# Kernel optimization log

Measured on AMD Instinct MI355X. Metric: run time of the kernel, lower is better.

The kernel has to match this reference:

```python
import jax, jax.numpy as jnp
import numpy as np

B, H, S, D = 8, 16, 1024, 64

def setup_inputs() -> dict:
    key = jax.random.key(0)
    kq, kk, kv, km = jax.random.split(key, 4)
    Q = jax.random.normal(kq, (B, H, S, D), dtype=jnp.float32)
    K = jax.random.normal(kk, (B, H, S, D), dtype=jnp.float32)
    V = jax.random.normal(kv, (B, H, S, D), dtype=jnp.float32)
    attn_mask = jax.random.randint(km, (B, H, S, S), 0, 2).astype(bool)
    return {"Q": Q, "K": K, "V": V, "attn_mask": attn_mask}

def reference(Q, K, V, attn_mask):
    # scores = Q @ K^T  (NOTE: source has no 1/sqrt(d) scaling)
    scores = jnp.einsum("bhqd,bhkd->bhqk", Q, K)
    # source uses masked_fill_(mask, 1e-9), i.e. masked positions become 1e-9 (not -inf)
    scores = jnp.where(attn_mask, jnp.float32(1e-9), scores)
    attn = jax.nn.softmax(scores, axis=-1)
    context = jnp.einsum("bhqk,bhkd->bhqd", attn, V)
    return context, attn
```

## Files before the change

### kernel.cpp

```cpp
#include <hip/hip_runtime.h>

#define Sn 1024
#define Dn 64
#define PH_LD 1032
#define K_LD 72
#define V_LD 72

typedef short v8s __attribute__((ext_vector_type(8)));
typedef unsigned short v8u __attribute__((ext_vector_type(8)));
typedef float v4f __attribute__((ext_vector_type(4)));
typedef int   v4i __attribute__((ext_vector_type(4)));

#define LGKM0()  asm volatile("s_waitcnt lgkmcnt(0)" ::: "memory")
#define SBAR()   do { asm volatile("" ::: "memory"); __builtin_amdgcn_s_barrier(); \
                      __builtin_amdgcn_sched_barrier(0); } while (0)

__device__ __forceinline__ unsigned short f2bf(float x) {
    union { float f; unsigned u; } v; v.f = x;
    return (unsigned short)((v.u + 0x7FFFu + ((v.u >> 16) & 1u)) >> 16);
}
__device__ __forceinline__ float bf2f(unsigned short h) {
    union { float f; unsigned u; } v; v.u = ((unsigned)h) << 16;
    return v.f;
}
__device__ __forceinline__ void split2(float x, unsigned short& h, unsigned short& l) {
    unsigned short hs = f2bf(x);
    h = hs; l = f2bf(x - bf2f(hs));
}

__global__ __launch_bounds__(256) void prep_kf(const float* __restrict__ K,
    unsigned short* __restrict__ KF)
{
    const int bh = blockIdx.x >> 4, kt = blockIdx.x & 15;
    const int t = threadIdx.x;
    const int w = t >> 6, lane = t & 63;
    const int fr = lane & 15, g = lane >> 4;
    const float* src = K + (((size_t)(bh << 10) + (kt << 6) + (w << 4) + fr) << 6);
    const v4f a0 = __builtin_nontemporal_load((const v4f*)(src + (g << 3)));
    const v4f a1 = __builtin_nontemporal_load((const v4f*)(src + (g << 3) + 4));
    const v4f b0 = __builtin_nontemporal_load((const v4f*)(src + 32 + (g << 3)));
    const v4f b1 = __builtin_nontemporal_load((const v4f*)(src + 32 + (g << 3) + 4));
    v8u h0, h1, l0, l1;
    #pragma unroll
    for (int j = 0; j < 4; ++j) {
        unsigned short hh, ll;
        split2(a0[j], hh, ll); h0[j] = hh;     l0[j] = ll;
        split2(a1[j], hh, ll); h0[4 + j] = hh; l0[4 + j] = ll;
        split2(b0[j], hh, ll); h1[j] = hh;     l1[j] = ll;
        split2(b1[j], hh, ll); h1[4 + j] = hh; l1[4 + j] = ll;
    }
    unsigned short* dst = KF + ((size_t)bh << 17) + ((size_t)((kt << 2) + w) << 11) + (lane << 3);
    *(v8u*)(dst)        = h0;
    *(v8u*)(dst + 512)  = h1;
    *(v8u*)(dst + 1024) = l0;
    *(v8u*)(dst + 1536) = l1;
}

__global__ __launch_bounds__(256) void prep_vf(const float* __restrict__ V,
    unsigned short* __restrict__ VF)
{
    __shared__ float Ts[64][65];
    const int bh = blockIdx.x >> 4, kt = blockIdx.x & 15;
    const int t = threadIdx.x;
    {
        const int r = t >> 2, cs = (t & 3) << 4;
        const float* src = V + ((size_t)bh * Sn + (kt << 6) + r) * Dn + cs;
        const v4f a = __builtin_nontemporal_load((const v4f*)src);
        const v4f b = __builtin_nontemporal_load((const v4f*)src + 1);
        const v4f c = __builtin_nontemporal_load((const v4f*)src + 2);
        const v4f d = __builtin_nontemporal_load((const v4f*)src + 3);
        #pragma unroll
        for (int j = 0; j < 4; ++j) {
            Ts[r][cs + j]      = a[j];
            Ts[r][cs + 4 + j]  = b[j];
            Ts[r][cs + 8 + j]  = c[j];
            Ts[r][cs + 12 + j] = d[j];
        }
    }
    __syncthreads();
    {
        const int w = t >> 6, lane = t & 63;
        const int fr = lane & 15, g = lane >> 4;
        const int d = (w << 4) + fr;
        unsigned short* dst = VF + ((size_t)bh << 16) + ((size_t)((kt << 2) + w) << 10) + (lane << 3);
        v8u o0, o1;
        #pragma unroll
        for (int j = 0; j < 8; ++j) o0[j] = f2bf(Ts[(g << 3) + j][d]);
        #pragma unroll
        for (int j = 0; j < 8; ++j) o1[j] = f2bf(Ts[32 + (g << 3) + j][d]);
        *(v8u*)dst         = o0;
        *(v8u*)(dst + 512) = o1;
    }
}

__global__ __launch_bounds__(256) void prep_m(const int* __restrict__ M,
    unsigned long long* __restrict__ MW)
{
    const int NW = 2097152;
    const int lane = threadIdx.x & 63;
    const int wave = (blockIdx.x << 2) + (threadIdx.x >> 6);
    const int nwaves = gridDim.x << 2;
    for (int w0 = wave << 3; w0 < NW; w0 += nwaves << 3) {
        unsigned long long b[8];
        #pragma unroll
        for (int s = 0; s < 8; ++s) {
            const int v = __builtin_nontemporal_load(&M[((size_t)(w0 + s) << 6) + lane]);
            b[s] = __ballot(v != 0);
        }
        if (lane == 0) {
            ulonglong2* dst = (ulonglong2*)(MW + w0);
            ulonglong2 p0, p1, p2, p3;
            p0.x = b[0]; p0.y = b[1]; p1.x = b[2]; p1.y = b[3];
            p2.x = b[4]; p2.y = b[5]; p3.x = b[6]; p3.y = b[7];
            dst[0] = p0; dst[1] = p1; dst[2] = p2; dst[3] = p3;
        }
    }
}

__global__ __launch_bounds__(256, 4) void fused_attn_c(
    const unsigned short* __restrict__ KFG, const unsigned short* __restrict__ VFG,
    const float* __restrict__ Q, const unsigned long long* __restrict__ MW,
    float* __restrict__ attnO, float* __restrict__ ctxO)
{
    __shared__ unsigned short Ph[16][PH_LD];
    __shared__ float rsumW[4][16];
    __shared__ float invL[16];

    const int tid  = threadIdx.x;
    const int lane = tid & 63;
    const int w    = tid >> 6;
    const int fr   = lane & 15;
    const int g    = lane >> 4;

    const int swz = ((blockIdx.x & 7) << 10) + (blockIdx.x >> 3);
    const int bh = swz >> 6;
    const int q0 = (swz & 63) << 4;

    const float* Qb = Q + (size_t)bh * Sn * Dn + (size_t)q0 * Dn;
    float*       Ab = attnO + (size_t)bh * Sn * Sn + (size_t)q0 * Sn;
    float*       Cb = ctxO  + (size_t)bh * Sn * Dn + (size_t)q0 * Dn;
    const unsigned short* KFb = KFG + ((size_t)bh << 17);
    const unsigned short* VFb = VFG + ((size_t)bh << 16);
    const unsigned long long* mwp = MW + ((size_t)bh << 14) + ((size_t)(q0 + fr) << 4);

    v8s qh0, qh1, ql0, ql1;
    {
        const float* qp = Qb + fr * Dn + (g << 3);
        float x0[8], x1[8];
        *(v4f*)&x0[0] = *(const v4f*)qp;
        *(v4f*)&x0[4] = *(const v4f*)(qp + 4);
        *(v4f*)&x1[0] = *(const v4f*)(qp + 32);
        *(v4f*)&x1[4] = *(const v4f*)(qp + 36);
        #pragma unroll
        for (int i = 0; i < 8; ++i) {
            unsigned short hh, ll;
            split2(x0[i], hh, ll); qh0[i] = (short)hh; ql0[i] = (short)ll;
            split2(x1[i], hh, ll); qh1[i] = (short)hh; ql1[i] = (short)ll;
        }
    }

    const int sh = (w << 4) + (g << 2);

#define LDK(kt, h0, h1, l0, l1) do {                                               \
        const unsigned short* _p = KFb + ((size_t)(((kt) << 2) + w) << 11) + (lane << 3); \
        h0 = *(const v8s*)_p;          h1 = *(const v8s*)(_p + 512);               \
        l0 = *(const v8s*)(_p + 1024); l1 = *(const v8s*)(_p + 1536);              \
    } while (0)

#define STEPA(h0, h1, l0, l1, mwv, kt) do {                                        \
        v4f acc = {0.f, 0.f, 0.f, 0.f};                                            \
        __builtin_amdgcn_s_setprio(1);                                             \
        acc = __builtin_amdgcn_mfma_f32_16x16x32_bf16(h0, qh0, acc, 0, 0, 0);      \
        acc = __builtin_amdgcn_mfma_f32_16x16x32_bf16(h1, qh1, acc, 0, 0, 0);      \
        acc = __builtin_amdgcn_mfma_f32_16x16x32_bf16(l0, qh0, acc, 0, 0, 0);      \
        acc = __builtin_amdgcn_mfma_f32_16x16x32_bf16(l1, qh1, acc, 0, 0, 0);      \
        acc = __builtin_amdgcn_mfma_f32_16x16x32_bf16(h0, ql0, acc, 0, 0, 0);      \
        acc = __builtin_amdgcn_mfma_f32_16x16x32_bf16(h1, ql1, acc, 0, 0, 0);      \
        __builtin_amdgcn_s_setprio(0);                                             \
        const unsigned mb = (unsigned)((mwv) >> sh);                               \
        const float e0 = (mb & 1u) ? 1.0f : __expf(acc[0]);                        \
        const float e1 = (mb & 2u) ? 1.0f : __expf(acc[1]);                        \
        const float e2 = (mb & 4u) ? 1.0f : __expf(acc[2]);                        \
        const float e3 = (mb & 8u) ? 1.0f : __expf(acc[3]);                        \
        rs += (e0 + e1) + (e2 + e3);                                               \
        ushort4 pk;                                                                \
        pk.x = f2bf(e0); pk.y = f2bf(e1); pk.z = f2bf(e2); pk.w = f2bf(e3);        \
        *(ushort4*)&Ph[fr][((kt) << 6) + (w << 4) + (g << 2)] = pk;                \
    } while (0)

    float rs = 0.f;

    {
        v8s ah0, ah1, al0, al1, bh0, bh1, bl0, bl1;
        LDK(0, ah0, ah1, al0, al1);
        LDK(1, bh0, bh1, bl0, bl1);
        unsigned long long mA = mwp[0], mB = mwp[1];
        for (int kt = 0; kt < 16; kt += 2) {
            const int k2 = (kt + 2 < 16) ? kt + 2 : kt;
            const int k3 = (kt + 3 < 16) ? kt + 3 : kt;
            v8s ch0, ch1, cl0, cl1, dh0, dh1, dl0, dl1;
            LDK(k2, ch0, ch1, cl0, cl1);
            LDK(k3, dh0, dh1, dl0, dl1);
            const unsigned long long mC = mwp[k2];
            const unsigned long long mD = mwp[k3];
            STEPA(ah0, ah1, al0, al1, mA, kt);
            STEPA(bh0, bh1, bl0, bl1, mB, kt + 1);
            ah0 = ch0; ah1 = ch1; al0 = cl0; al1 = cl1; mA = mC;
            bh0 = dh0; bh1 = dh1; bl0 = dl0; bl1 = dl1; mB = mD;
        }
    }

    rs += __shfl_xor(rs, 16);
    rs += __shfl_xor(rs, 32);
    if (g == 0) rsumW[w][fr] = rs;
    __builtin_amdgcn_sched_barrier(0);
    LGKM0();
    SBAR();
    if (tid < 16) {
        const float s = rsumW[0][tid] + rsumW[1][tid] + rsumW[2][tid] + rsumW[3][tid];
        invL[tid] = 1.0f / s;
    }
    __builtin_amdgcn_sched_barrier(0);
    LGKM0();
    SBAR();

#define LDV(kt, v0, v1) do {                                                       \
        const unsigned short* _p = VFb + ((size_t)(((kt) << 2) + w) << 10) + (lane << 3); \
        v0 = *(const v8s*)_p;  v1 = *(const v8s*)(_p + 512);                       \
    } while (0)

#define STEPB(v0, v1, kt) do {                                                     \
        const v8s a0 = *(const v8s*)&Ph[fr][((kt) << 6) + (g << 3)];               \
        const v8s a1 = *(const v8s*)&Ph[fr][((kt) << 6) + 32 + (g << 3)];          \
        __builtin_amdgcn_s_setprio(1);                                             \
        accp = __builtin_amdgcn_mfma_f32_16x16x32_bf16(a0, v0, accp, 0, 0, 0);     \
        accp = __builtin_amdgcn_mfma_f32_16x16x32_bf16(a1, v1, accp, 0, 0, 0);     \
        __builtin_amdgcn_s_setprio(0);                                             \
    } while (0)

    v8s va0, va1, vb0, vb1;
    LDV(0, va0, va1);
    LDV(1, vb0, vb1);

    {
        const int qq = tid >> 4, ii = tid & 15;
        const float inv = invL[qq];
        float* arow = Ab + (size_t)qq * Sn;
        #pragma unroll
        for (int c = 0; c < 16; ++c) {
            const int k0 = (c << 6) + (ii << 2);
            const ushort4 p = *(const ushort4*)&Ph[qq][k0];
            v4f o;
            o[0] = bf2f(p.x) * inv; o[1] = bf2f(p.y) * inv;
            o[2] = bf2f(p.z) * inv; o[3] = bf2f(p.w) * inv;
            __builtin_nontemporal_store(o, (v4f*)(arow + k0));
        }
    }

    const int dcol = (w << 4) + fr;
    v4f accp = {0.f, 0.f, 0.f, 0.f};
    for (int kt = 0; kt < 16; kt += 2) {
        const int k2 = (kt + 2 < 16) ? kt + 2 : kt;
        const int k3 = (kt + 3 < 16) ? kt + 3 : kt;
        v8s vc0, vc1, vd0, vd1;
        LDV(k2, vc0, vc1);
        LDV(k3, vd0, vd1);
        STEPB(va0, va1, kt);
        STEPB(vb0, vb1, kt + 1);
        va0 = vc0; va1 = vc1;
        vb0 = vd0; vb1 = vd1;
    }
    #pragma unroll
    for (int r = 0; r < 4; ++r) {
        const int q = (g << 2) + r;
        __builtin_nontemporal_store(accp[r] * invL[q], &Cb[(size_t)q * Dn + dcol]);
    }
#undef LDK
#undef STEPA
#undef LDV
#undef STEPB
}

__global__ __launch_bounds__(256, 3) void fused_attn_fb(
    const float* __restrict__ Q, const float* __restrict__ K,
    const float* __restrict__ V, const int* __restrict__ M,
    float* __restrict__ attnO, float* __restrict__ ctxO)
{
    __shared__ unsigned short Ph[16][1048];
    __shared__ __align__(16) unsigned short Kraw[2 * 64 * K_LD];
    __shared__ float rsumW[4][16];
    __shared__ float invL[16];

    unsigned short (*Khi)[K_LD] = (unsigned short (*)[K_LD])Kraw;
    unsigned short (*Klo)[K_LD] = (unsigned short (*)[K_LD])(Kraw + 64 * K_LD);
    unsigned short (*Vt)[V_LD]  = (unsigned short (*)[V_LD])Kraw;

    const int tid  = threadIdx.x;
    const int lane = tid & 63;
    const int w    = tid >> 6;
    const int fr   = lane & 15;
    const int g    = lane >> 4;

    const int bh = blockIdx.x >> 6;
    const int q0 = (blockIdx.x & 63) << 4;

    const float* Qb = Q + (size_t)bh * Sn * Dn + (size_t)q0 * Dn;
    const float* Kb = K + (size_t)bh * Sn * Dn;
    const float* Vb = V + (size_t)bh * Sn * Dn;
    const int*   Mb = M + (size_t)bh * Sn * Sn + (size_t)q0 * Sn;
    float*       Ab = attnO + (size_t)bh * Sn * Sn + (size_t)q0 * Sn;
    float*       Cb = ctxO  + (size_t)bh * Sn * Dn + (size_t)q0 * Dn;

    v8s qh0, qh1, ql0, ql1;
    {
        const float* qp = Qb + fr * Dn + (g << 3);
        float x0[8], x1[8];
        *(v4f*)&x0[0] = *(const v4f*)qp;
        *(v4f*)&x0[4] = *(const v4f*)(qp + 4);
        *(v4f*)&x1[0] = *(const v4f*)(qp + 32);
        *(v4f*)&x1[4] = *(const v4f*)(qp + 36);
        #pragma unroll
        for (int i = 0; i < 8; ++i) {
            unsigned short hh, ll;
            split2(x0[i], hh, ll); qh0[i] = (short)hh; ql0[i] = (short)ll;
            split2(x1[i], hh, ll); qh1[i] = (short)hh; ql1[i] = (short)ll;
        }
    }

    const int srow = tid >> 4;
    const int sc4  = (tid & 15) << 2;

    const int* mp = Mb + (size_t)fr * Sn + (w << 4) + (g << 2);
    v4i mv = *(const v4i*)mp;

    v4f ka[4];
    #pragma unroll
    for (int i = 0; i < 4; ++i)
        ka[i] = *(const v4f*)(Kb + (size_t)(srow + (i << 4)) * Dn + sc4);

    float rs = 0.f;

    for (int kt = 0; kt < 16; ++kt) {
        __syncthreads();
        v4f kb[4];
        if (kt < 15) {
            const float* kn = Kb + (size_t)((kt + 1) << 6) * Dn;
            #pragma unroll
            for (int i = 0; i < 4; ++i)
                kb[i] = *(const v4f*)(kn + (size_t)(srow + (i << 4)) * Dn + sc4);
        }
        v4i mnext = mv;
        if (kt < 15) mnext = *(const v4i*)(mp + ((kt + 1) << 6));

        #pragma unroll
        for (int i = 0; i < 4; ++i) {
            const int row = srow + (i << 4);
            ushort4 hv, lv;
            split2(ka[i][0], hv.x, lv.x); split2(ka[i][1], hv.y, lv.y);
            split2(ka[i][2], hv.z, lv.z); split2(ka[i][3], hv.w, lv.w);
            *(ushort4*)&Khi[row][sc4] = hv;
            *(ushort4*)&Klo[row][sc4] = lv;
        }
        __syncthreads();

        const int krow = (w << 4) + fr;
        const v8s kh0 = *(const v8s*)&Khi[krow][(g << 3)];
        const v8s kh1 = *(const v8s*)&Khi[krow][32 + (g << 3)];
        const v8s kl0 = *(const v8s*)&Klo[krow][(g << 3)];
        const v8s kl1 = *(const v8s*)&Klo[krow][32 + (g << 3)];

        v4f acc = {0.f, 0.f, 0.f, 0.f};
        acc = __builtin_amdgcn_mfma_f32_16x16x32_bf16(kh0, qh0, acc, 0, 0, 0);
        acc = __builtin_amdgcn_mfma_f32_16x16x32_bf16(kh1, qh1, acc, 0, 0, 0);
        acc = __builtin_amdgcn_mfma_f32_16x16x32_bf16(kl0, qh0, acc, 0, 0, 0);
        acc = __builtin_amdgcn_mfma_f32_16x16x32_bf16(kl1, qh1, acc, 0, 0, 0);
        acc = __builtin_amdgcn_mfma_f32_16x16x32_bf16(kh0, ql0, acc, 0, 0, 0);
        acc = __builtin_amdgcn_mfma_f32_16x16x32_bf16(kh1, ql1, acc, 0, 0, 0);

        const float e0 = mv[0] ? 1.0f : __expf(acc[0]);
        const float e1 = mv[1] ? 1.0f : __expf(acc[1]);
        const float e2 = mv[2] ? 1.0f : __expf(acc[2]);
        const float e3 = mv[3] ? 1.0f : __expf(acc[3]);
        rs += (e0 + e1) + (e2 + e3);
        ushort4 pk;
        pk.x = f2bf(e0); pk.y = f2bf(e1); pk.z = f2bf(e2); pk.w = f2bf(e3);
        *(ushort4*)&Ph[fr][(kt << 6) + (w << 4) + (g << 2)] = pk;

        mv = mnext;
        #pragma unroll
        for (int i = 0; i < 4; ++i) ka[i] = kb[i];
    }

    rs += __shfl_xor(rs, 16);
    rs += __shfl_xor(rs, 32);
    if (g == 0) rsumW[w][fr] = rs;
    __syncthreads();
    if (tid < 16) {
        const float s = rsumW[0][tid] + rsumW[1][tid] + rsumW[2][tid] + rsumW[3][tid];
        invL[tid] = 1.0f / s;
    }
    __syncthreads();

    const int dcol = (w << 4) + fr;
    v4f va[4];
    #pragma unroll
    for (int i = 0; i < 4; ++i)
        va[i] = *(const v4f*)(Vb + (size_t)(srow + (i << 4)) * Dn + sc4);

    v4f accp = {0.f, 0.f, 0.f, 0.f};
    for (int kt = 0; kt < 16; ++kt) {
        __syncthreads();
        v4f vb[4];
        if (kt < 15) {
            const float* vn = Vb + (size_t)((kt + 1) << 6) * Dn;
            #pragma unroll
            for (int i = 0; i < 4; ++i)
                vb[i] = *(const v4f*)(vn + (size_t)(srow + (i << 4)) * Dn + sc4);
        }
        #pragma unroll
        for (int i = 0; i < 4; ++i) {
            const int row = srow + (i << 4);
            Vt[sc4 + 0][row] = f2bf(va[i][0]);
            Vt[sc4 + 1][row] = f2bf(va[i][1]);
            Vt[sc4 + 2][row] = f2bf(va[i][2]);
            Vt[sc4 + 3][row] = f2bf(va[i][3]);
        }
        __syncthreads();

        #pragma unroll
        for (int c = 0; c < 2; ++c) {
            const int kc = (kt << 6) + (c << 5);
            const v8s a = *(const v8s*)&Ph[fr][kc + (g << 3)];
            const v8s b = *(const v8s*)&Vt[dcol][(c << 5) + (g << 3)];
            accp = __builtin_amdgcn_mfma_f32_16x16x32_bf16(a, b, accp, 0, 0, 0);
        }
        #pragma unroll
        for (int i = 0; i < 4; ++i) va[i] = vb[i];
    }
    #pragma unroll
    for (int r = 0; r < 4; ++r) {
        const int q = (g << 2) + r;
        Cb[(size_t)q * Dn + dcol] = accp[r] * invL[q];
    }

    {
        const int qq = tid >> 4, ii = tid & 15;
        const float inv = invL[qq];
        float* arow = Ab + (size_t)qq * Sn;
        #pragma unroll
        for (int c = 0; c < 16; ++c) {
            const int k0 = (c << 6) + (ii << 2);
            const ushort4 p = *(const ushort4*)&Ph[qq][k0];
            v4f o;
            o[0] = bf2f(p.x) * inv; o[1] = bf2f(p.y) * inv;
            o[2] = bf2f(p.z) * inv; o[3] = bf2f(p.w) * inv;
            *(v4f*)(arow + k0) = o;
        }
    }
}

extern "C" void kernel_launch(void* const* d_in, const int* in_sizes, int n_in,
                              void* d_out, int out_size, void* d_ws, size_t ws_size,
                              hipStream_t stream) {
    const float* Q    = (const float*)d_in[0];
    const float* K    = (const float*)d_in[1];
    const float* V    = (const float*)d_in[2];
    const int*   mask = (const int*)d_in[3];

    float* ctx  = (float*)d_out;
    float* attn = (float*)d_out + (size_t)128 * Sn * Dn;

    const size_t NELEM = (size_t)128 * Sn * Dn;
    const size_t MWORDS = (size_t)128 * Sn * 16;
    const size_t NEED  = NELEM * 2 * 3 + MWORDS * 8;

    if (ws_size >= NEED) {
        unsigned short* KF = (unsigned short*)d_ws;
        unsigned short* VF = KF + NELEM * 2;
        unsigned long long* MWp = (unsigned long long*)((char*)d_ws + NELEM * 2 * 3);
        prep_kf<<<2048, 256, 0, stream>>>(K, KF);
        prep_vf<<<2048, 256, 0, stream>>>(V, VF);
        prep_m<<<2048, 256, 0, stream>>>(mask, MWp);
        fused_attn_c<<<128 * 64, 256, 0, stream>>>(KF, VF, Q, MWp, attn, ctx);
    } else {
        fused_attn_fb<<<128 * 64, 256, 0, stream>>>(Q, K, V, mask, attn, ctx);
    }
}
```

Measured before the change: 293.3 us.

## Replace split-bf16 QK^T with single fp16 MFMA and deeper K prefetch

Drops the three-term bf16 hi/lo split for Q·K^T and uses plain fp16 operands with two f16 MFMAs per tile instead of six. This halves the K workspace and its traffic and cuts QK matrix work by about three times. The K loop is also restructured into a fully unrolled four-deep register prefetch ring. The risk is lower accuracy: fp16 has fewer mantissa bits than the split representation and can overflow for large inputs, and unscaled scores feed exp directly.

After: 263.5 us. 10.2% less time.

```diff
diff --git a/kernel.cpp b/kernel.cpp
--- a/kernel.cpp
+++ b/kernel.cpp
@@ -8,6 +8,7 @@
 
 typedef short v8s __attribute__((ext_vector_type(8)));
 typedef unsigned short v8u __attribute__((ext_vector_type(8)));
+typedef _Float16 v8h __attribute__((ext_vector_type(8)));
 typedef float v4f __attribute__((ext_vector_type(4)));
 typedef int   v4i __attribute__((ext_vector_type(4)));
 
@@ -28,7 +29,7 @@
     h = hs; l = f2bf(x - bf2f(hs));
 }
 
-__global__ __launch_bounds__(256) void prep_kf(const float* __restrict__ K,
+__global__ __launch_bounds__(256) void prep_kh(const float* __restrict__ K,
     unsigned short* __restrict__ KF)
 {
     const int bh = blockIdx.x >> 4, kt = blockIdx.x & 15;
@@ -40,20 +41,15 @@
     const v4f a1 = __builtin_nontemporal_load((const v4f*)(src + (g << 3) + 4));
     const v4f b0 = __builtin_nontemporal_load((const v4f*)(src + 32 + (g << 3)));
     const v4f b1 = __builtin_nontemporal_load((const v4f*)(src + 32 + (g << 3) + 4));
-    v8u h0, h1, l0, l1;
+    v8h c0, c1;
     #pragma unroll
     for (int j = 0; j < 4; ++j) {
-        unsigned short hh, ll;
-        split2(a0[j], hh, ll); h0[j] = hh;     l0[j] = ll;
-        split2(a1[j], hh, ll); h0[4 + j] = hh; l0[4 + j] = ll;
-        split2(b0[j], hh, ll); h1[j] = hh;     l1[j] = ll;
-        split2(b1[j], hh, ll); h1[4 + j] = hh; l1[4 + j] = ll;
-    }
-    unsigned short* dst = KF + ((size_t)bh << 17) + ((size_t)((kt << 2) + w) << 11) + (lane << 3);
-    *(v8u*)(dst)        = h0;
-    *(v8u*)(dst + 512)  = h1;
-    *(v8u*)(dst + 1024) = l0;
-    *(v8u*)(dst + 1536) = l1;
+        c0[j] = (_Float16)a0[j]; c0[4 + j] = (_Float16)a1[j];
+        c1[j] = (_Float16)b0[j]; c1[4 + j] = (_Float16)b1[j];
+    }
+    unsigned short* dst = KF + ((size_t)bh << 16) + ((size_t)((kt << 2) + w) << 10) + (lane << 3);
+    *(v8h*)(dst)       = c0;
+    *(v8h*)(dst + 512) = c1;
 }
 
 __global__ __launch_bounds__(256) void prep_vf(const float* __restrict__ V,
@@ -117,7 +113,7 @@
     }
 }
 
-__global__ __launch_bounds__(256, 4) void fused_attn_c(
+__global__ __launch_bounds__(256, 4) void fused_attn_f(
     const unsigned short* __restrict__ KFG, const unsigned short* __restrict__ VFG,
     const float* __restrict__ Q, const unsigned long long* __restrict__ MW,
     float* __restrict__ attnO, float* __restrict__ ctxO)
@@ -139,43 +135,36 @@
     const float* Qb = Q + (size_t)bh * Sn * Dn + (size_t)q0 * Dn;
     float*       Ab = attnO + (size_t)bh * Sn * Sn + (size_t)q0 * Sn;
     float*       Cb = ctxO  + (size_t)bh * Sn * Dn + (size_t)q0 * Dn;
-    const unsigned short* KFb = KFG + ((size_t)bh << 17);
+    const unsigned short* KFb = KFG + ((size_t)bh << 16);
     const unsigned short* VFb = VFG + ((size_t)bh << 16);
     const unsigned long long* mwp = MW + ((size_t)bh << 14) + ((size_t)(q0 + fr) << 4);
 
-    v8s qh0, qh1, ql0, ql1;
+    v8h qf0, qf1;
     {
         const float* qp = Qb + fr * Dn + (g << 3);
-        float x0[8], x1[8];
-        *(v4f*)&x0[0] = *(const v4f*)qp;
-        *(v4f*)&x0[4] = *(const v4f*)(qp + 4);
-        *(v4f*)&x1[0] = *(const v4f*)(qp + 32);
-        *(v4f*)&x1[4] = *(const v4f*)(qp + 36);
-        #pragma unroll
-        for (int i = 0; i < 8; ++i) {
-            unsigned short hh, ll;
-            split2(x0[i], hh, ll); qh0[i] = (short)hh; ql0[i] = (short)ll;
-            split2(x1[i], hh, ll); qh1[i] = (short)hh; ql1[i] = (short)ll;
+        const v4f x0a = *(const v4f*)qp;
+        const v4f x0b = *(const v4f*)(qp + 4);
+        const v4f x1a = *(const v4f*)(qp + 32);
+        const v4f x1b = *(const v4f*)(qp + 36);
+        #pragma unroll
+        for (int j = 0; j < 4; ++j) {
+            qf0[j] = (_Float16)x0a[j]; qf0[4 + j] = (_Float16)x0b[j];
+            qf1[j] = (_Float16)x1a[j]; qf1[4 + j] = (_Float16)x1b[j];
         }
     }
 
     const int sh = (w << 4) + (g << 2);
 
-#define LDK(kt, h0, h1, l0, l1) do {                                               \
-        const unsigned short* _p = KFb + ((size_t)(((kt) << 2) + w) << 11) + (lane << 3); \
-        h0 = *(const v8s*)_p;          h1 = *(const v8s*)(_p + 512);               \
-        l0 = *(const v8s*)(_p + 1024); l1 = *(const v8s*)(_p + 1536);              \
+#define LDK(kt, k0_, k1_) do {                                                     \
+        const unsigned short* _p = KFb + ((size_t)(((kt) << 2) + w) << 10) + (lane << 3); \
+        k0_ = *(const v8h*)_p;  k1_ = *(const v8h*)(_p + 512);                     \
     } while (0)
 
-#define STEPA(h0, h1, l0, l1, mwv, kt) do {                                        \
+#define STEPA(k0_, k1_, mwv, kt) do {                                              \
         v4f acc = {0.f, 0.f, 0.f, 0.f};                                            \
         __builtin_amdgcn_s_setprio(1);                                             \
-        acc = __builtin_amdgcn_mfma_f32_16x16x32_bf16(h0, qh0, acc, 0, 0, 0);      \
-        acc = __builtin_amdgcn_mfma_f32_16x16x32_bf16(h1, qh1, acc, 0, 0, 0);      \
-        acc = __builtin_amdgcn_mfma_f32_16x16x32_bf16(l0, qh0, acc, 0, 0, 0);      \
-        acc = __builtin_amdgcn_mfma_f32_16x16x32_bf16(l1, qh1, acc, 0, 0, 0);      \
-        acc = __builtin_amdgcn_mfma_f32_16x16x32_bf16(h0, ql0, acc, 0, 0, 0);      \
-        acc = __builtin_amdgcn_mfma_f32_16x16x32_bf16(h1, ql1, acc, 0, 0, 0);      \
+        acc = __builtin_amdgcn_mfma_f32_16x16x32_f16(k0_, qf0, acc, 0, 0, 0);      \
+        acc = __builtin_amdgcn_mfma_f32_16x16x32_f16(k1_, qf1, acc, 0, 0, 0);      \
         __builtin_amdgcn_s_setprio(0);                                             \
         const unsigned mb = (unsigned)((mwv) >> sh);                               \
         const float e0 = (mb & 1u) ? 1.0f : __expf(acc[0]);                        \
@@ -191,22 +180,20 @@
     float rs = 0.f;
 
     {
-        v8s ah0, ah1, al0, al1, bh0, bh1, bl0, bl1;
-        LDK(0, ah0, ah1, al0, al1);
-        LDK(1, bh0, bh1, bl0, bl1);
-        unsigned long long mA = mwp[0], mB = mwp[1];
-        for (int kt = 0; kt < 16; kt += 2) {
-            const int k2 = (kt + 2 < 16) ? kt + 2 : kt;
-            const int k3 = (kt + 3 < 16) ? kt + 3 : kt;
-            v8s ch0, ch1, cl0, cl1, dh0, dh1, dl0, dl1;
-            LDK(k2, ch0, ch1, cl0, cl1);
-            LDK(k3, dh0, dh1, dl0, dl1);
-            const unsigned long long mC = mwp[k2];
-            const unsigned long long mD = mwp[k3];
-            STEPA(ah0, ah1, al0, al1, mA, kt);
-            STEPA(bh0, bh1, bl0, bl1, mB, kt + 1);
-            ah0 = ch0; ah1 = ch1; al0 = cl0; al1 = cl1; mA = mC;
-            bh0 = dh0; bh1 = dh1; bl0 = dl0; bl1 = dl1; mB = mD;
+        v8h k0s[4], k1s[4];
+        unsigned long long mk[4];
+        LDK(0, k0s[0], k1s[0]);
+        LDK(1, k0s[1], k1s[1]);
+        LDK(2, k0s[2], k1s[2]);
+        LDK(3, k0s[3], k1s[3]);
+        mk[0] = mwp[0]; mk[1] = mwp[1]; mk[2] = mwp[2]; mk[3] = mwp[3];
+        #pragma unroll
+        for (int kt = 0; kt < 16; ++kt) {
+            STEPA(k0s[kt & 3], k1s[kt & 3], mk[kt & 3], kt);
+            if (kt + 4 < 16) {
+                LDK(kt + 4, k0s[kt & 3], k1s[kt & 3]);
+                mk[kt & 3] = mwp[kt + 4];
+            }
         }
     }
 
@@ -224,17 +211,17 @@
     LGKM0();
     SBAR();
 
-#define LDV(kt, v0, v1) do {                                                       \
+#define LDV(kt, v0_, v1_) do {                                                     \
         const unsigned short* _p = VFb + ((size_t)(((kt) << 2) + w) << 10) + (lane << 3); \
-        v0 = *(const v8s*)_p;  v1 = *(const v8s*)(_p + 512);                       \
+        v0_ = *(const v8s*)_p;  v1_ = *(const v8s*)(_p + 512);                     \
     } while (0)
 
-#define STEPB(v0, v1, kt) do {                                                     \
+#define STEPB(v0_, v1_, kt) do {                                                   \
         const v8s a0 = *(const v8s*)&Ph[fr][((kt) << 6) + (g << 3)];               \
         const v8s a1 = *(const v8s*)&Ph[fr][((kt) << 6) + 32 + (g << 3)];          \
         __builtin_amdgcn_s_setprio(1);                                             \
-        accp = __builtin_amdgcn_mfma_f32_16x16x32_bf16(a0, v0, accp, 0, 0, 0);     \
-        accp = __builtin_amdgcn_mfma_f32_16x16x32_bf16(a1, v1, accp, 0, 0, 0);     \
+        accp = __builtin_amdgcn_mfma_f32_16x16x32_bf16(a0, v0_, accp, 0, 0, 0);    \
+        accp = __builtin_amdgcn_mfma_f32_16x16x32_bf16(a1, v1_, accp, 0, 0, 0);    \
         __builtin_amdgcn_s_setprio(0);                                             \
     } while (0)
 
@@ -472,16 +459,16 @@
 
     const size_t NELEM = (size_t)128 * Sn * Dn;
     const size_t MWORDS = (size_t)128 * Sn * 16;
-    const size_t NEED  = NELEM * 2 * 3 + MWORDS * 8;
+    const size_t NEED  = NELEM * 4 + MWORDS * 8;
 
     if (ws_size >= NEED) {
         unsigned short* KF = (unsigned short*)d_ws;
-        unsigned short* VF = KF + NELEM * 2;
-        unsigned long long* MWp = (unsigned long long*)((char*)d_ws + NELEM * 2 * 3);
-        prep_kf<<<2048, 256, 0, stream>>>(K, KF);
+        unsigned short* VF = KF + NELEM;
+        unsigned long long* MWp = (unsigned long long*)((char*)d_ws + NELEM * 4);
+        prep_kh<<<2048, 256, 0, stream>>>(K, KF);
         prep_vf<<<2048, 256, 0, stream>>>(V, VF);
         prep_m<<<2048, 256, 0, stream>>>(mask, MWp);
-        fused_attn_c<<<128 * 64, 256, 0, stream>>>(KF, VF, Q, MWp, attn, ctx);
+        fused_attn_f<<<128 * 64, 256, 0, stream>>>(KF, VF, Q, MWp, attn, ctx);
     } else {
         fused_attn_fb<<<128 * 64, 256, 0, stream>>>(Q, K, V, mask, attn, ctx);
     }
```
